# Performance work log

Hardware: AMD Instinct MI355X
Metric: run time of the kernel (lower is better)

## Reference

```python
import jax, jax.numpy as jnp
from jax import lax
import numpy as np

B, T, C, H = 2048, 1024, 9, 36  # batch, seq_len, input_size, hidden_size


def setup_inputs() -> dict:
    key = jax.random.key(0)
    ks = jax.random.split(key, 4)
    x = jax.random.normal(ks[0], (B, T, C), dtype=jnp.float32)
    # torch GRU param shapes: weight_ih (3H, C), weight_hh (3H, H), biases (3H,)
    w_ih = jax.random.normal(ks[1], (3 * H, C), dtype=jnp.float32) * (1.0 / np.sqrt(C))
    w_hh = jax.random.normal(ks[2], (3 * H, H), dtype=jnp.float32) * (1.0 / np.sqrt(H))
    b_ih = jnp.zeros((3 * H,), dtype=jnp.float32)
    b_hh = jnp.zeros((3 * H,), dtype=jnp.float32)
    w_head = jax.random.normal(ks[3], (1, H), dtype=jnp.float32) * (1.0 / np.sqrt(H))
    b_head = jnp.zeros((1,), dtype=jnp.float32)
    return {"x": x, "w_ih": w_ih, "w_hh": w_hh, "b_ih": b_ih, "b_hh": b_hh,
            "w_head": w_head, "b_head": b_head}


def reference(x, w_ih, w_hh, b_ih, b_hh, w_head, b_head):
    """TinyGRUInt8.forward in fp32 (Quant/DeQuant stubs are identity).
    GRU (batch_first, torch gate order r,z,n), take last timestep, Linear head.
    """
    h = w_hh.shape[1]
    # Precompute input contribution to all gates for every timestep: (B,T,3H)
    gx = jnp.einsum('btc,gc->btg', x, w_ih) + b_ih
    gx = jnp.moveaxis(gx, 1, 0)  # (T,B,3H) for scan over time

    def step(h_prev, gxt):
        gh = h_prev @ w_hh.T + b_hh                      # (B,3H)
        r = jax.nn.sigmoid(gxt[:, :h] + gh[:, :h])
        z = jax.nn.sigmoid(gxt[:, h:2 * h] + gh[:, h:2 * h])
        n = jnp.tanh(gxt[:, 2 * h:] + r * gh[:, 2 * h:])
        h_new = (1.0 - z) * n + z * h_prev
        return h_new, None

    h0 = jnp.zeros((x.shape[0], h), dtype=x.dtype)
    h_last, _ = lax.scan(step, h0, gx)                   # last output == final hidden
    return h_last @ w_head.T + b_head                    # (B,1)
```

## Files before the change

### kernel.cpp

```cpp
#include <hip/hip_runtime.h>

typedef float     v2f __attribute__((ext_vector_type(2)));
typedef _Float16  v2h __attribute__((ext_vector_type(2)));
typedef unsigned int uint;

#define BB 2048
#define TT 1024
#define CC 9
#define HH 36
#define G3 108
#define CSTEPS 32
#define CF (CSTEPS * CC)
#define FS 12
#define GXS 112
#define NCH (TT / CSTEPS)

__device__ __forceinline__ void lds_fence() {
    asm volatile("" ::: "memory");
    __builtin_amdgcn_sched_barrier(0);
}

__device__ __forceinline__ void pinh(v2h& v) {
    uint t = __builtin_bit_cast(uint, v);
    asm volatile("" : "+v"(t));
    v = __builtin_bit_cast(v2h, t);
}

__device__ __forceinline__ void gload4(const float* g, float* l) {
    __builtin_amdgcn_global_load_lds(
        (const __attribute__((address_space(1))) unsigned int*)g,
        (__attribute__((address_space(3))) unsigned int*)l,
        4, 0, 0);
}

__global__ __launch_bounds__(64)
__attribute__((amdgpu_waves_per_eu(2, 2)))
void gru_kernel(
    const float* __restrict__ x,
    const float* __restrict__ w_ih,
    const float* __restrict__ w_hh,
    const float* __restrict__ b_ih,
    const float* __restrict__ b_hh,
    const float* __restrict__ w_head,
    const float* __restrict__ b_head,
    float* __restrict__ out)
{
    const int b = blockIdx.x;
    const int l = threadIdx.x;

    __shared__ __align__(16) float    fstage[CSTEPS * FS];
    __shared__ __align__(16) float    gxbuf[CSTEPS * GXS];
    __shared__ __align__(16) float    ahbuf[128];
    __shared__ __align__(16) _Float16 hbuf[40];

    const int i0 = (2 * l     < G3) ? 2 * l     : G3 - 1;
    const int i1 = (2 * l + 1 < G3) ? 2 * l + 1 : G3 - 1;

    v2h wh0[18], wh1[18];
    float bB0, bB1;
    {
        const float* p0 = w_hh + (size_t)i0 * HH;
        const float* p1 = w_hh + (size_t)i1 * HH;
#pragma unroll
        for (int k = 0; k < 18; ++k) {
            wh0[k] = (v2h){(_Float16)p0[2*k], (_Float16)p0[2*k+1]};
            wh1[k] = (v2h){(_Float16)p1[2*k], (_Float16)p1[2*k+1]};
        }
        const bool n0 = i0 >= 2 * HH, n1 = i1 >= 2 * HH;
        bB0 = n0 ? b_hh[i0] : 0.f;
        bB1 = n1 ? b_hh[i1] : 0.f;
    }
#pragma unroll
    for (int k = 0; k < 18; ++k) { pinh(wh0[k]); pinh(wh1[k]); }
    asm volatile("" : "+v"(bB0), "+v"(bB1));

    v2f wx0[4], wx1[4];
    float w80, w81, bA0, bA1;
    {
        const float* q0 = w_ih + (size_t)i0 * CC;
        const float* q1 = w_ih + (size_t)i1 * CC;
#pragma unroll
        for (int p = 0; p < 4; ++p) {
            wx0[p] = (v2f){q0[2*p], q0[2*p+1]};
            wx1[p] = (v2f){q1[2*p], q1[2*p+1]};
        }
        w80 = q0[8];
        w81 = q1[8];
        const bool n0 = i0 >= 2 * HH, n1 = i1 >= 2 * HH;
        bA0 = n0 ? b_ih[i0] : (b_ih[i0] + b_hh[i0]);
        bA1 = n1 ? b_ih[i1] : (b_ih[i1] + b_hh[i1]);
    }

    int offk[6];
#pragma unroll
    for (int k = 0; k < 6; ++k) {
        int idx = k * 64 + l;
        int s   = idx / 12;
        int q   = idx - 12 * s;
        offk[k] = s * 9 + (q < 9 ? q : 8);
    }

    const float* xg = x + (size_t)b * (TT * CC);

#pragma unroll
    for (int k = 0; k < 6; ++k) gload4(xg + offk[k], &fstage[k * 64]);

    v2h h2[18];
#pragma unroll
    for (int k = 0; k < 18; ++k) h2[k] = (v2h){(_Float16)0.f, (_Float16)0.f};
    float h_own = 0.f;

    for (int c = 0; c < NCH; ++c) {
        asm volatile("s_waitcnt vmcnt(0)" ::: "memory");
        __builtin_amdgcn_sched_barrier(0);

        for (int s = 0; s < CSTEPS; ++s) {
            float4 xa = *(const float4*)&fstage[s * FS];
            float4 xc = *(const float4*)&fstage[s * FS + 4];
            float  x8 = fstage[s * FS + 8];
            v2f X0 = (v2f){xa.x, xa.y};
            v2f X1 = (v2f){xa.z, xa.w};
            v2f X2 = (v2f){xc.x, xc.y};
            v2f X3 = (v2f){xc.z, xc.w};
            v2f a0 = (v2f){bA0, 0.f};
            v2f a1 = (v2f){bA1, 0.f};
            a0 = __builtin_elementwise_fma(wx0[0], X0, a0);
            a1 = __builtin_elementwise_fma(wx1[0], X0, a1);
            a0 = __builtin_elementwise_fma(wx0[1], X1, a0);
            a1 = __builtin_elementwise_fma(wx1[1], X1, a1);
            a0 = __builtin_elementwise_fma(wx0[2], X2, a0);
            a1 = __builtin_elementwise_fma(wx1[2], X2, a1);
            a0 = __builtin_elementwise_fma(wx0[3], X3, a0);
            a1 = __builtin_elementwise_fma(wx1[3], X3, a1);
            float ax0 = fmaf(w80, x8, a0.x + a0.y);
            float ax1 = fmaf(w81, x8, a1.x + a1.y);
            if (l < 54) *(v2f*)&gxbuf[s * GXS + 2 * l] = (v2f){ax0, ax1};
        }
        lds_fence();

        if (c + 1 < NCH) {
            const float* src = xg + (size_t)(c + 1) * CF;
#pragma unroll
            for (int k = 0; k < 6; ++k) gload4(src + offk[k], &fstage[k * 64]);
        }

        for (int s = 0; s < CSTEPS; ++s) {
            float a0a = bB0, a1a = bB1, a0b = 0.f, a1b = 0.f;
#pragma unroll
            for (int k = 0; k < 9; ++k) {
                a0a = __builtin_amdgcn_fdot2(wh0[k],     h2[k],     a0a, false);
                a1a = __builtin_amdgcn_fdot2(wh1[k],     h2[k],     a1a, false);
                a0b = __builtin_amdgcn_fdot2(wh0[k + 9], h2[k + 9], a0b, false);
                a1b = __builtin_amdgcn_fdot2(wh1[k + 9], h2[k + 9], a1b, false);
            }
            float ah0 = a0a + a0b;
            float ah1 = a1a + a1b;

            *(v2f*)&ahbuf[2 * l] = (v2f){ah0, ah1};
            lds_fence();

            if (l < HH) {
                float gxr = gxbuf[s * GXS + l];
                float gxz = gxbuf[s * GXS + HH + l];
                float gxn = gxbuf[s * GXS + 2 * HH + l];
                float ahr = ahbuf[l];
                float ahz = ahbuf[HH + l];
                float ahn = ahbuf[2 * HH + l];
                float sr = gxr + ahr;
                float sz = gxz + ahz;
                float r = __builtin_amdgcn_rcpf(1.f + __expf(-sr));
                float z = __builtin_amdgcn_rcpf(1.f + __expf(-sz));
                float a = gxn + r * ahn;
                float n = 1.f - 2.f * __builtin_amdgcn_rcpf(__expf(2.f * a) + 1.f);
                h_own = z * (h_own - n) + n;
                hbuf[l] = (_Float16)h_own;
            }
            lds_fence();

#pragma unroll
            for (int q = 0; q < 4; ++q) {
                uint4 t4 = ((const uint4*)hbuf)[q];
                h2[4*q+0] = __builtin_bit_cast(v2h, t4.x);
                h2[4*q+1] = __builtin_bit_cast(v2h, t4.y);
                h2[4*q+2] = __builtin_bit_cast(v2h, t4.z);
                h2[4*q+3] = __builtin_bit_cast(v2h, t4.w);
            }
            {
                uint2 t2 = ((const uint2*)hbuf)[8];
                h2[16] = __builtin_bit_cast(v2h, t2.x);
                h2[17] = __builtin_bit_cast(v2h, t2.y);
            }
        }
    }

    float whead = (l < HH) ? w_head[l] : 0.f;
    float v = (l < HH) ? h_own * whead : 0.f;
#pragma unroll
    for (int off = 32; off; off >>= 1) v += __shfl_down(v, off);
    if (l == 0) out[b] = v + b_head[0];
}

extern "C" void kernel_launch(void* const* d_in, const int* in_sizes, int n_in,
                              void* d_out, int out_size, void* d_ws, size_t ws_size,
                              hipStream_t stream) {
    const float* x      = (const float*)d_in[0];
    const float* w_ih   = (const float*)d_in[1];
    const float* w_hh   = (const float*)d_in[2];
    const float* b_ih   = (const float*)d_in[3];
    const float* b_hh   = (const float*)d_in[4];
    const float* w_head = (const float*)d_in[5];
    const float* b_head = (const float*)d_in[6];
    float* out = (float*)d_out;

    gru_kernel<<<BB, 64, 0, stream>>>(x, w_ih, w_hh, b_ih, b_hh,
                                      w_head, b_head, out);
}
```

Before: 412.7 us.

## Compute all three gates per hidden unit in-lane and broadcast h via readlane

```diff
diff --git a/kernel.cpp b/kernel.cpp
--- a/kernel.cpp
+++ b/kernel.cpp
@@ -11,7 +11,7 @@
 #define G3 108
 #define CSTEPS 32
 #define CF (CSTEPS * CC)
-#define FS 12
+#define FPAD 320
 #define GXS 112
 #define NCH (TT / CSTEPS)
 
@@ -48,66 +48,56 @@
     const int b = blockIdx.x;
     const int l = threadIdx.x;
 
-    __shared__ __align__(16) float    fstage[CSTEPS * FS];
-    __shared__ __align__(16) float    gxbuf[CSTEPS * GXS];
-    __shared__ __align__(16) float    ahbuf[128];
-    __shared__ __align__(16) _Float16 hbuf[40];
+    __shared__ __align__(16) float fstage[FPAD];
+    __shared__ __align__(16) float gxbuf[CSTEPS * GXS];
 
+    const int u = (l < HH) ? l : HH - 1;
     const int i0 = (2 * l     < G3) ? 2 * l     : G3 - 1;
     const int i1 = (2 * l + 1 < G3) ? 2 * l + 1 : G3 - 1;
 
-    v2h wh0[18], wh1[18];
-    float bB0, bB1;
+    v2h whr[18], whz[18], whn[18];
+    float bnh;
     {
-        const float* p0 = w_hh + (size_t)i0 * HH;
-        const float* p1 = w_hh + (size_t)i1 * HH;
+        const float* pr = w_hh + (size_t)u * HH;
+        const float* pz = w_hh + (size_t)(HH + u) * HH;
+        const float* pn = w_hh + (size_t)(2 * HH + u) * HH;
 #pragma unroll
         for (int k = 0; k < 18; ++k) {
-            wh0[k] = (v2h){(_Float16)p0[2*k], (_Float16)p0[2*k+1]};
-            wh1[k] = (v2h){(_Float16)p1[2*k], (_Float16)p1[2*k+1]};
+            whr[k] = (v2h){(_Float16)pr[2*k], (_Float16)pr[2*k+1]};
+            whz[k] = (v2h){(_Float16)pz[2*k], (_Float16)pz[2*k+1]};
+            whn[k] = (v2h){(_Float16)pn[2*k], (_Float16)pn[2*k+1]};
         }
-        const bool n0 = i0 >= 2 * HH, n1 = i1 >= 2 * HH;
-        bB0 = n0 ? b_hh[i0] : 0.f;
-        bB1 = n1 ? b_hh[i1] : 0.f;
+        bnh = b_hh[2 * HH + u];
     }
 #pragma unroll
-    for (int k = 0; k < 18; ++k) { pinh(wh0[k]); pinh(wh1[k]); }
-    asm volatile("" : "+v"(bB0), "+v"(bB1));
+    for (int k = 0; k < 18; ++k) { pinh(whr[k]); pinh(whz[k]); pinh(whn[k]); }
+    asm volatile("" : "+v"(bnh));
 
-    v2f wx0[4], wx1[4];
-    float w80, w81, bA0, bA1;
+    float wxa[CC], wxb[CC], bA0, bA1;
     {
         const float* q0 = w_ih + (size_t)i0 * CC;
         const float* q1 = w_ih + (size_t)i1 * CC;
 #pragma unroll
-        for (int p = 0; p < 4; ++p) {
-            wx0[p] = (v2f){q0[2*p], q0[2*p+1]};
-            wx1[p] = (v2f){q1[2*p], q1[2*p+1]};
-        }
-        w80 = q0[8];
-        w81 = q1[8];
+        for (int q = 0; q < CC; ++q) { wxa[q] = q0[q]; wxb[q] = q1[q]; }
         const bool n0 = i0 >= 2 * HH, n1 = i1 >= 2 * HH;
         bA0 = n0 ? b_ih[i0] : (b_ih[i0] + b_hh[i0]);
         bA1 = n1 ? b_ih[i1] : (b_ih[i1] + b_hh[i1]);
     }
 
-    int offk[6];
+    int offs[5];
 #pragma unroll
-    for (int k = 0; k < 6; ++k) {
+    for (int k = 0; k < 5; ++k) {
         int idx = k * 64 + l;
-        int s   = idx / 12;
-        int q   = idx - 12 * s;
-        offk[k] = s * 9 + (q < 9 ? q : 8);
+        offs[k] = (idx < CF) ? idx : (CF - 1);
     }
 
     const float* xg = x + (size_t)b * (TT * CC);
+#pragma unroll
+    for (int k = 0; k < 5; ++k) gload4(xg + offs[k], &fstage[k * 64]);
 
+    v2h h2s[18];
 #pragma unroll
-    for (int k = 0; k < 6; ++k) gload4(xg + offk[k], &fstage[k * 64]);
-
-    v2h h2[18];
-#pragma unroll
-    for (int k = 0; k < 18; ++k) h2[k] = (v2h){(_Float16)0.f, (_Float16)0.f};
+    for (int k = 0; k < 18; ++k) h2s[k] = (v2h){(_Float16)0.f, (_Float16)0.f};
     float h_own = 0.f;
 
     for (int c = 0; c < NCH; ++c) {
@@ -115,81 +105,60 @@
         __builtin_amdgcn_sched_barrier(0);
 
         for (int s = 0; s < CSTEPS; ++s) {
-            float4 xa = *(const float4*)&fstage[s * FS];
-            float4 xc = *(const float4*)&fstage[s * FS + 4];
-            float  x8 = fstage[s * FS + 8];
-            v2f X0 = (v2f){xa.x, xa.y};
-            v2f X1 = (v2f){xa.z, xa.w};
-            v2f X2 = (v2f){xc.x, xc.y};
-            v2f X3 = (v2f){xc.z, xc.w};
-            v2f a0 = (v2f){bA0, 0.f};
-            v2f a1 = (v2f){bA1, 0.f};
-            a0 = __builtin_elementwise_fma(wx0[0], X0, a0);
-            a1 = __builtin_elementwise_fma(wx1[0], X0, a1);
-            a0 = __builtin_elementwise_fma(wx0[1], X1, a0);
-            a1 = __builtin_elementwise_fma(wx1[1], X1, a1);
-            a0 = __builtin_elementwise_fma(wx0[2], X2, a0);
-            a1 = __builtin_elementwise_fma(wx1[2], X2, a1);
-            a0 = __builtin_elementwise_fma(wx0[3], X3, a0);
-            a1 = __builtin_elementwise_fma(wx1[3], X3, a1);
-            float ax0 = fmaf(w80, x8, a0.x + a0.y);
-            float ax1 = fmaf(w81, x8, a1.x + a1.y);
-            if (l < 54) *(v2f*)&gxbuf[s * GXS + 2 * l] = (v2f){ax0, ax1};
+            const float* xs = &fstage[s * CC];
+            float a0 = bA0, a1 = bA1;
+#pragma unroll
+            for (int q = 0; q < CC; ++q) {
+                float xv = xs[q];
+                a0 = fmaf(wxa[q], xv, a0);
+                a1 = fmaf(wxb[q], xv, a1);
+            }
+            if (l < 54) *(v2f*)&gxbuf[s * GXS + 2 * l] = (v2f){a0, a1};
         }
         lds_fence();
 
         if (c + 1 < NCH) {
             const float* src = xg + (size_t)(c + 1) * CF;
 #pragma unroll
-            for (int k = 0; k < 6; ++k) gload4(src + offk[k], &fstage[k * 64]);
+            for (int k = 0; k < 5; ++k) gload4(src + offs[k], &fstage[k * 64]);
         }
 
+#pragma unroll 2
         for (int s = 0; s < CSTEPS; ++s) {
-            float a0a = bB0, a1a = bB1, a0b = 0.f, a1b = 0.f;
+            float gxr = gxbuf[s * GXS + u];
+            float gxz = gxbuf[s * GXS + HH + u];
+            float gxn = gxbuf[s * GXS + 2 * HH + u];
+
+            float r0 = 0.f, r1 = 0.f, z0 = 0.f, z1 = 0.f, n0 = bnh, n1 = 0.f;
 #pragma unroll
             for (int k = 0; k < 9; ++k) {
-                a0a = __builtin_amdgcn_fdot2(wh0[k],     h2[k],     a0a, false);
-                a1a = __builtin_amdgcn_fdot2(wh1[k],     h2[k],     a1a, false);
-                a0b = __builtin_amdgcn_fdot2(wh0[k + 9], h2[k + 9], a0b, false);
-                a1b = __builtin_amdgcn_fdot2(wh1[k + 9], h2[k + 9], a1b, false);
+                r0 = __builtin_amdgcn_fdot2(whr[k],     h2s[k],     r0, false);
+                z0 = __builtin_amdgcn_fdot2(whz[k],     h2s[k],     z0, false);
+                n0 = __builtin_amdgcn_fdot2(whn[k],     h2s[k],     n0, false);
+                r1 = __builtin_amdgcn_fdot2(whr[k + 9], h2s[k + 9], r1, false);
+                z1 = __builtin_amdgcn_fdot2(whz[k + 9], h2s[k + 9], z1, false);
+                n1 = __builtin_amdgcn_fdot2(whn[k + 9], h2s[k + 9], n1, false);
             }
-            float ah0 = a0a + a0b;
-            float ah1 = a1a + a1b;
+            float sr = gxr + (r0 + r1);
+            float sz = gxz + (z0 + z1);
+            float gh = n0 + n1;
 
-            *(v2f*)&ahbuf[2 * l] = (v2f){ah0, ah1};
-            lds_fence();
+            float r = __builtin_amdgcn_rcpf(1.f + __expf(-sr));
+            float z = __builtin_amdgcn_rcpf(1.f + __expf(-sz));
+            float a = gxn + r * gh;
+            float n = 1.f - 2.f * __builtin_amdgcn_rcpf(__expf(2.f * a) + 1.f);
+            h_own = z * (h_own - n) + n;
 
-            if (l < HH) {
-                float gxr = gxbuf[s * GXS + l];
-                float gxz = gxbuf[s * GXS + HH + l];
-                float gxn = gxbuf[s * GXS + 2 * HH + l];
-                float ahr = ahbuf[l];
-                float ahz = ahbuf[HH + l];
-                float ahn = ahbuf[2 * HH + l];
-                float sr = gxr + ahr;
-                float sz = gxz + ahz;
-                float r = __builtin_amdgcn_rcpf(1.f + __expf(-sr));
-                float z = __builtin_amdgcn_rcpf(1.f + __expf(-sz));
-                float a = gxn + r * ahn;
-                float n = 1.f - 2.f * __builtin_amdgcn_rcpf(__expf(2.f * a) + 1.f);
-                h_own = z * (h_own - n) + n;
-                hbuf[l] = (_Float16)h_own;
-            }
-            lds_fence();
-
+            float nb = __builtin_bit_cast(float,
+                __builtin_amdgcn_mov_dpp(__builtin_bit_cast(int, h_own),
+                                         0xB1, 0xF, 0xF, true));
+            uint lo = (uint)__builtin_bit_cast(unsigned short, (_Float16)h_own);
+            uint hi = (uint)__builtin_bit_cast(unsigned short, (_Float16)nb);
+            uint hw = lo | (hi << 16);
 #pragma unroll
-            for (int q = 0; q < 4; ++q) {
-                uint4 t4 = ((const uint4*)hbuf)[q];
-                h2[4*q+0] = __builtin_bit_cast(v2h, t4.x);
-                h2[4*q+1] = __builtin_bit_cast(v2h, t4.y);
-                h2[4*q+2] = __builtin_bit_cast(v2h, t4.z);
-                h2[4*q+3] = __builtin_bit_cast(v2h, t4.w);
-            }
-            {
-                uint2 t2 = ((const uint2*)hbuf)[8];
-                h2[16] = __builtin_bit_cast(v2h, t2.x);
-                h2[17] = __builtin_bit_cast(v2h, t2.y);
-            }
+            for (int k = 0; k < 18; ++k)
+                h2s[k] = __builtin_bit_cast(v2h,
+                             __builtin_amdgcn_readlane(hw, 2 * k));
         }
     }
 
```

Measured after the change: 481.7 us. 16.7% more time.
